# Kernel tuning notes

Measured on AMD Instinct MI355X. Metric: run time of the kernel, lower is better.

Reference implementation:

```python
import jax, jax.numpy as jnp
import numpy as np

NUM_HEADS = 16


def setup_inputs() -> dict:
    key = jax.random.key(0)
    ks = jax.random.split(key, 7)
    B, S, H = 4, 2048, 1024
    scale = 1.0 / np.sqrt(H)
    return {
        "hidden_states": jax.random.normal(ks[0], (B, S, H), dtype=jnp.float32),
        "attention_mask": jnp.ones((B, S), dtype=jnp.int32),
        "Wq": jax.random.normal(ks[1], (H, H), dtype=jnp.float32) * scale,
        "bq": jnp.zeros((H,), dtype=jnp.float32),
        "Wk": jax.random.normal(ks[2], (H, H), dtype=jnp.float32) * scale,
        "bk": jnp.zeros((H,), dtype=jnp.float32),
        "Wv": jax.random.normal(ks[3], (H, H), dtype=jnp.float32) * scale,
        "bv": jnp.zeros((H,), dtype=jnp.float32),
    }


def _split_heads(x, n_heads):
    B, S, H = x.shape
    return x.reshape(B, S, n_heads, H // n_heads).transpose(0, 2, 1, 3)  # [B,h,S,d]


def reference(hidden_states, attention_mask, Wq, bq, Wk, bk, Wv, bv):
    B, S, H = hidden_states.shape
    dh = H // NUM_HEADS
    # nn.Linear applies x @ W.T + b
    q = _split_heads(hidden_states @ Wq.T + bq, NUM_HEADS)
    k = _split_heads(hidden_states @ Wk.T + bk, NUM_HEADS)
    v = _split_heads(hidden_states @ Wv.T + bv, NUM_HEADS)
    scores = jnp.einsum("bhqd,bhkd->bhqk", q, k)  # [B,h,S,S]
    # masked_fill with -inf before scaling == masking after scaling
    mask = attention_mask[:, None, None, :] == 0
    scores = jnp.where(mask, -jnp.inf, scores)
    probs = jax.nn.softmax(scores / jnp.sqrt(jnp.float32(dh)), axis=-1)
    out = jnp.einsum("bhqk,bhkd->bhqd", probs, v)  # [B,h,S,d]
    return out.transpose(0, 2, 1, 3).reshape(B, S, H)
```

## Files before the change

### kernel.cpp

```cpp
#include <hip/hip_runtime.h>
#include <hip/hip_bf16.h>
#include <stdint.h>

constexpr int CB  = 4;
constexpr int CS  = 2048;
constexpr int CH  = 1024;
constexpr int CNH = 16;
constexpr int CDH = 64;
constexpr int CM  = CB * CS;

typedef __bf16 bf16x8 __attribute__((ext_vector_type(8)));
typedef float  f32x4  __attribute__((ext_vector_type(4)));

__device__ __forceinline__ unsigned short f2bf(float f) {
    union { float f; unsigned u; } c; c.f = f;
    unsigned u = c.u;
    unsigned r = (u + 0x7fffu + ((u >> 16) & 1u)) >> 16;
    return (unsigned short)r;
}

__device__ __forceinline__ void gl_lds16(const void* g, void* l) {
    __builtin_amdgcn_global_load_lds((const __attribute__((address_space(1))) uint32_t*)g,
                                     (__attribute__((address_space(3))) uint32_t*)l,
                                     16, 0, 0);
}

__device__ __forceinline__ float fexp2(float x) {
#if __has_builtin(__builtin_amdgcn_exp2f)
    return __builtin_amdgcn_exp2f(x);
#else
    return exp2f(x);
#endif
}

__device__ __forceinline__ unsigned vperm(unsigned s0, unsigned s1, unsigned sel) {
#if __has_builtin(__builtin_amdgcn_perm)
    return __builtin_amdgcn_perm(s0, s1, sel);
#else
    unsigned r = 0;
    for (int k = 0; k < 4; k++) {
        unsigned idx = (sel >> (8 * k)) & 0xff;
        unsigned byte = (idx < 4) ? (s1 >> (8 * idx)) : (s0 >> (8 * (idx - 4)));
        r |= (byte & 0xff) << (8 * k);
    }
    return r;
#endif
}
__device__ __forceinline__ unsigned pack_hihalf(unsigned lo_u, unsigned hi_u) {
    return vperm(hi_u, lo_u, 0x07060302u);
}

constexpr float C_SC = 0.125f * 1.44269504f;

__global__ __launch_bounds__(256) void cvt_all(const float* __restrict__ hs,
                                               const float* __restrict__ w0,
                                               const float* __restrict__ w1,
                                               const float* __restrict__ w2,
                                               unsigned short* __restrict__ Xb,
                                               unsigned short* __restrict__ Wb) {
    int z = blockIdx.y;
    const float* src; unsigned short* dst; int n4;
    if (z == 0)      { src = hs; dst = Xb;              n4 = CM * CH / 4; }
    else if (z == 1) { src = w0; dst = Wb;              n4 = CH * CH / 4; }
    else if (z == 2) { src = w1; dst = Wb + CH * CH;    n4 = CH * CH / 4; }
    else             { src = w2; dst = Wb + 2 * CH * CH; n4 = CH * CH / 4; }
    int i = blockIdx.x * blockDim.x + threadIdx.x;
    if (i < n4) {
        float4 v = ((const float4*)src)[i];
        ushort4 o;
        o.x = f2bf(v.x); o.y = f2bf(v.y); o.z = f2bf(v.z); o.w = f2bf(v.w);
        ((ushort4*)dst)[i] = o;
    }
}

__global__ __launch_bounds__(256) void qkv_gemm(
    const unsigned short* __restrict__ Xb,
    const unsigned short* __restrict__ Wb,
    const float* __restrict__ bq, const float* __restrict__ bk, const float* __restrict__ bv,
    unsigned short* __restrict__ Qo,
    unsigned short* __restrict__ Ko,
    unsigned short* __restrict__ Vt)
{
    __shared__ alignas(16) unsigned char smem[34816];
    typedef unsigned short (*tile_t)[128][32];
    tile_t As = (tile_t)smem;
    tile_t Bs = (tile_t)(smem + 16384);
    typedef unsigned short (*ep_t)[136];
    ep_t Ep = (ep_t)smem;

    const int tid  = threadIdx.x;
    const int wave = tid >> 6, lane = tid & 63;
    const int wm = wave >> 1, wn = wave & 1;
    const int col = lane & 15, quad = lane >> 4;
    const int gm = blockIdx.x * 128, gn = blockIdx.y * 128;
    const int z  = blockIdx.z;
    const unsigned short* W = Wb + (size_t)z * CH * CH;

    f32x4 zero = {0.f, 0.f, 0.f, 0.f};
    f32x4 acc[4][4];
    for (int i = 0; i < 4; i++) for (int j = 0; j < 4; j++) acc[i][j] = zero;

    const int arow = lane >> 2;
    const int acol = (lane & 3) * 8;

    auto stage = [&](int buf, int k0) {
        for (int c = 0; c < 2; ++c) {
            int r0 = wave * 32 + c * 16;
            gl_lds16(Xb + (size_t)(gm + r0 + arow) * CH + k0 + acol, &As[buf][r0][0]);
            gl_lds16(W  + (size_t)(gn + r0 + arow) * CH + k0 + acol, &Bs[buf][r0][0]);
        }
    };

    stage(0, 0);
    for (int kk = 0; kk < 32; ++kk) {
        int cur = kk & 1;
        __syncthreads();
        if (kk < 31) stage(cur ^ 1, (kk + 1) * 32);
        bf16x8 af[4], bfm[4];
        for (int i = 0; i < 4; i++)
            af[i] = *(const bf16x8*)&As[cur][wm * 64 + i * 16 + col][quad * 8];
        for (int j = 0; j < 4; j++)
            bfm[j] = *(const bf16x8*)&Bs[cur][wn * 64 + j * 16 + col][quad * 8];
        for (int i = 0; i < 4; i++)
            for (int j = 0; j < 4; j++)
                acc[i][j] = __builtin_amdgcn_mfma_f32_16x16x32_bf16(af[i], bfm[j], acc[i][j], 0, 0, 0);
    }

    __syncthreads();

    const float* bias = (z == 0) ? bq : (z == 1) ? bk : bv;
    const int bb = gm >> 11, ss0 = gm & 2047;
    const int h0 = gn >> 6;

    if (z == 2) {
        for (int j = 0; j < 4; j++) {
            int nl = wn * 64 + j * 16 + col;
            float bias_v = bias[gn + nl];
            for (int i = 0; i < 4; i++) {
                int ml = wm * 64 + i * 16 + quad * 4;
                unsigned d0 = (unsigned)f2bf(acc[i][j][0] + bias_v) |
                              ((unsigned)f2bf(acc[i][j][1] + bias_v) << 16);
                unsigned d1 = (unsigned)f2bf(acc[i][j][2] + bias_v) |
                              ((unsigned)f2bf(acc[i][j][3] + bias_v) << 16);
                *(unsigned*)&Ep[nl][ml]     = d0;
                *(unsigned*)&Ep[nl][ml + 2] = d1;
            }
        }
        __syncthreads();
        for (int p = 0; p < 8; p++) {
            int nl = p * 16 + (tid >> 4);
            int seg = tid & 15;
            uint4 v = *(const uint4*)&Ep[nl][seg * 8];
            int h = h0 + (nl >> 6), d = nl & 63;
            *(uint4*)(Vt + ((size_t)(bb * CNH + h) * CDH + d) * CS + ss0 + seg * 8) = v;
        }
    } else {
        const float mulf = (z == 0) ? C_SC : 1.0f;
        for (int j = 0; j < 4; j++) {
            int nl = wn * 64 + j * 16 + col;
            float bias_v = bias[gn + nl];
            for (int i = 0; i < 4; i++)
                for (int r = 0; r < 4; r++) {
                    int ml = wm * 64 + i * 16 + quad * 4 + r;
                    Ep[ml][nl] = f2bf((acc[i][j][r] + bias_v) * mulf);
                }
        }
        __syncthreads();
        unsigned short* dst01 = (z == 0) ? Qo : Ko;
        for (int p = 0; p < 8; p++) {
            int ml = p * 16 + (tid >> 4);
            int half = (tid >> 3) & 1, seg = tid & 7;
            uint4 v = *(const uint4*)&Ep[ml][half * 64 + seg * 8];
            int h = h0 + half;
            *(uint4*)(dst01 + ((size_t)(bb * CNH + h) * CS + ss0 + ml) * CDH + seg * 8) = v;
        }
    }
}

__global__ __launch_bounds__(256, 2) void flash_attn(
    const unsigned short* __restrict__ Q,
    const unsigned short* __restrict__ K,
    const unsigned short* __restrict__ Vt,
    const int* __restrict__ mask,
    float* __restrict__ out)
{
    __shared__ alignas(16) unsigned short Ks[2][64][64];
    __shared__ alignas(16) unsigned short Vs[2][64][64];
    __shared__ alignas(16) unsigned int   Ps[4][64][32];
    __shared__ unsigned int Mbits[64];

    const int tid  = threadIdx.x;
    const int wave = tid >> 6, lane = tid & 63;
    const int col = lane & 15, quad = lane >> 4;
    const int bh = blockIdx.y;
    const int bI = bh >> 4, hI = bh & 15;
    const int q0 = blockIdx.x * 256 + wave * 64;

    const unsigned short* Qp = Q  + (size_t)bh * CS * CDH;
    const unsigned short* Kp = K  + (size_t)bh * CS * CDH;
    const unsigned short* Vp = Vt + (size_t)bh * CDH * CS;

    {
        const int* mg = mask + bI * CS;
        for (int j = 0; j < 8; j++) {
            int idx = wave * 512 + j * 64 + lane;
            unsigned long long bal = __ballot(mg[idx] != 0);
            if (lane == 0) {
                Mbits[wave * 16 + j * 2]     = (unsigned int)bal;
                Mbits[wave * 16 + j * 2 + 1] = (unsigned int)(bal >> 32);
            }
        }
    }

    bf16x8 aq[4][2];
    for (int i = 0; i < 4; i++)
        for (int ks = 0; ks < 2; ks++)
            aq[i][ks] = *(const bf16x8*)(Qp + (size_t)(q0 + i * 16 + col) * CDH + ks * 32 + quad * 8);

    bf16x8 onesb;
    {
        union { unsigned short u; __bf16 b; } ob; ob.u = 0x3F80;
        for (int j = 0; j < 8; j++) onesb[j] = ob.b;
    }

    f32x4 zero = {0.f, 0.f, 0.f, 0.f};
    f32x4 o[4][4], lfr[4];
    for (int i = 0; i < 4; i++) {
        lfr[i] = zero;
        for (int id = 0; id < 4; id++) o[i][id] = zero;
    }

    const int srow = lane >> 3;
    const int schk = (lane & 7) ^ srow;

    auto stageKV = [&](int buf, int t) {
        const unsigned short* kg = Kp + (size_t)t * 64 * CDH;
        for (int c = 0; c < 2; c++) {
            int r0 = wave * 16 + c * 8;
            gl_lds16(kg + (size_t)(r0 + srow) * CDH + schk * 8, &Ks[buf][r0][0]);
            gl_lds16(Vp + (size_t)(r0 + srow) * CS + t * 64 + schk * 8, &Vs[buf][r0][0]);
        }
    };

    stageKV(0, 0);
    for (int kt = 0; kt < 32; ++kt) {
        int cur = kt & 1;
        __syncthreads();
        if (kt < 31) stageKV(cur ^ 1, kt + 1);

        f32x4 sfr[4][4];
        for (int i = 0; i < 4; i++) for (int ik = 0; ik < 4; ik++) sfr[i][ik] = zero;
        for (int ks = 0; ks < 2; ks++) {
            bf16x8 bkf[4];
            for (int ik = 0; ik < 4; ik++)
                bkf[ik] = *(const bf16x8*)&Ks[cur][ik * 16 + col][((ks * 4 + quad) ^ (col & 7)) * 8];
            for (int i = 0; i < 4; i++)
                for (int ik = 0; ik < 4; ik++)
                    sfr[i][ik] = __builtin_amdgcn_mfma_f32_16x16x32_bf16(aq[i][ks], bkf[ik], sfr[i][ik], 0, 0, 0);
        }

        unsigned int w0 = Mbits[kt * 2], w1 = Mbits[kt * 2 + 1];
        if ((w0 & w1) != 0xFFFFFFFFu) {
            float madd[4];
            madd[0] = ((w0 >> col) & 1u)        ? 0.f : -1.0e30f;
            madd[1] = ((w0 >> (col + 16)) & 1u) ? 0.f : -1.0e30f;
            madd[2] = ((w1 >> col) & 1u)        ? 0.f : -1.0e30f;
            madd[3] = ((w1 >> (col + 16)) & 1u) ? 0.f : -1.0e30f;
            for (int i = 0; i < 4; i++)
                for (int ik = 0; ik < 4; ik++)
                    for (int r = 0; r < 4; r++)
                        sfr[i][ik][r] += madd[ik];
        }

        for (int i = 0; i < 4; i++)
            for (int ik = 0; ik < 2; ik++)
                for (int r = 0; r < 4; r++) {
                    union { float f; unsigned u; } a, b;
                    a.f = fexp2(sfr[i][ik][r]);
                    b.f = fexp2(sfr[i][ik + 2][r]);
                    unsigned dw = pack_hihalf(a.u, b.u);
                    int row = i * 16 + quad * 4 + r;
                    int p = ik * 16 + col;
                    Ps[wave][row][(((p >> 2) ^ (row & 7)) << 2) + (p & 3)] = dw;
                }

        for (int i = 0; i < 4; i++) {
            const unsigned* base = &Ps[wave][i * 16 + col][0];
            uint4 w0v = *(const uint4*)(base + (((quad * 2 + 0) ^ (col & 7)) << 2));
            uint4 w1v = *(const uint4*)(base + (((quad * 2 + 1) ^ (col & 7)) << 2));
            uint4 lo, hi;
            lo.x = vperm(w0v.y, w0v.x, 0x05040100u); hi.x = vperm(w0v.y, w0v.x, 0x07060302u);
            lo.y = vperm(w0v.w, w0v.z, 0x05040100u); hi.y = vperm(w0v.w, w0v.z, 0x07060302u);
            lo.z = vperm(w1v.y, w1v.x, 0x05040100u); hi.z = vperm(w1v.y, w1v.x, 0x07060302u);
            lo.w = vperm(w1v.w, w1v.z, 0x05040100u); hi.w = vperm(w1v.w, w1v.z, 0x07060302u);
            bf16x8 ap0, ap1;
            __builtin_memcpy(&ap0, &lo, 16);
            __builtin_memcpy(&ap1, &hi, 16);

            for (int ks = 0; ks < 2; ks++) {
                bf16x8 ap = (ks == 0) ? ap0 : ap1;
                bf16x8 bvf[4];
                for (int id = 0; id < 4; id++)
                    bvf[id] = *(const bf16x8*)&Vs[cur][id * 16 + col][((ks * 4 + quad) ^ (col & 7)) * 8];
                for (int id = 0; id < 4; id++)
                    o[i][id] = __builtin_amdgcn_mfma_f32_16x16x32_bf16(ap, bvf[id], o[i][id], 0, 0, 0);
                lfr[i] = __builtin_amdgcn_mfma_f32_16x16x32_bf16(ap, onesb, lfr[i], 0, 0, 0);
            }
        }
    }

    for (int i = 0; i < 4; i++)
        for (int r = 0; r < 4; r++) {
            int sI = q0 + i * 16 + quad * 4 + r;
            float inv = 1.0f / lfr[i][r];
            for (int id = 0; id < 4; id++)
                out[((size_t)(bI * CS + sI)) * CH + hI * CDH + id * 16 + col] = o[i][id][r] * inv;
        }
}

extern "C" void kernel_launch(void* const* d_in, const int* in_sizes, int n_in,
                              void* d_out, int out_size, void* d_ws, size_t ws_size,
                              hipStream_t stream) {
    const float* hs  = (const float*)d_in[0];
    const int*  mask = (const int*)d_in[1];
    const float* Wq  = (const float*)d_in[2];
    const float* bq  = (const float*)d_in[3];
    const float* Wk  = (const float*)d_in[4];
    const float* bk  = (const float*)d_in[5];
    const float* Wv  = (const float*)d_in[6];
    const float* bv  = (const float*)d_in[7];
    float* out = (float*)d_out;

    char* ws = (char*)d_ws;
    unsigned short* Xb = (unsigned short*)(ws);
    unsigned short* Wb = (unsigned short*)(ws + 16777216);
    unsigned short* Qb = (unsigned short*)(ws + 23068672);
    unsigned short* Kb = (unsigned short*)(ws + 39845888);
    unsigned short* Vt = (unsigned short*)(ws + 56623104);

    cvt_all<<<dim3(8192, 4), 256, 0, stream>>>(hs, Wq, Wk, Wv, Xb, Wb);

    qkv_gemm<<<dim3(CM / 128, CH / 128, 3), 256, 0, stream>>>(Xb, Wb, bq, bk, bv, Qb, Kb, Vt);

    flash_attn<<<dim3(CS / 256, CB * CNH), 256, 0, stream>>>(Qb, Kb, Vt, mask, out);
}
```

Measured before the change: 262.9 us.

## Transpose QK^T MFMA and build P operand in registers via permlane swaps

The QK^T MFMA operands are swapped so the score tile comes out transposed, with kv indices along rows. Each lane can then pack exp2 results with v_cvt_pk_bf16 and redistribute them with permlane32/16 swaps into the A-operand layout for the PV MFMA. This removes the per-wave LDS round trip through the Ps buffer and the vperm repacking, and frees its shared memory. It also hoists V fragment loads and adds s_setprio around MFMA bursts, at the cost of extra register pressure and reliance on the gfx950 permlane builtins or their slower fallbacks.

Result: faster. 253.6 us (-3.6%).

```diff
diff --git a/kernel.cpp b/kernel.cpp
--- a/kernel.cpp
+++ b/kernel.cpp
@@ -33,21 +33,38 @@
 #endif
 }
 
-__device__ __forceinline__ unsigned vperm(unsigned s0, unsigned s1, unsigned sel) {
-#if __has_builtin(__builtin_amdgcn_perm)
-    return __builtin_amdgcn_perm(s0, s1, sel);
+__device__ __forceinline__ unsigned cvtpk_bf16(float lo, float hi) {
+    unsigned r;
+    asm("v_cvt_pk_bf16_f32 %0, %1, %2" : "=v"(r) : "v"(lo), "v"(hi));
+    return r;
+}
+
+__device__ __forceinline__ void pl32swap(unsigned &a, unsigned &b) {
+#if __has_builtin(__builtin_amdgcn_permlane32_swap)
+    auto r = __builtin_amdgcn_permlane32_swap(a, b, false, false);
+    a = r[0]; b = r[1];
 #else
-    unsigned r = 0;
-    for (int k = 0; k < 4; k++) {
-        unsigned idx = (sel >> (8 * k)) & 0xff;
-        unsigned byte = (idx < 4) ? (s1 >> (8 * idx)) : (s0 >> (8 * (idx - 4)));
-        r |= (byte & 0xff) << (8 * k);
-    }
-    return r;
+    int lane = threadIdx.x & 63;
+    unsigned as = (unsigned)__shfl((int)a, lane ^ 32);
+    unsigned bs = (unsigned)__shfl((int)b, lane ^ 32);
+    unsigned na = (lane < 32) ? a : bs;
+    unsigned nb = (lane < 32) ? as : b;
+    a = na; b = nb;
 #endif
 }
-__device__ __forceinline__ unsigned pack_hihalf(unsigned lo_u, unsigned hi_u) {
-    return vperm(hi_u, lo_u, 0x07060302u);
+
+__device__ __forceinline__ void pl16swap(unsigned &a, unsigned &b) {
+#if __has_builtin(__builtin_amdgcn_permlane16_swap)
+    auto r = __builtin_amdgcn_permlane16_swap(a, b, false, false);
+    a = r[0]; b = r[1];
+#else
+    unsigned as = __builtin_amdgcn_ds_swizzle(a, 0x401F);
+    unsigned bs = __builtin_amdgcn_ds_swizzle(b, 0x401F);
+    int odd = (threadIdx.x >> 4) & 1;
+    unsigned na = odd ? bs : a;
+    unsigned nb = odd ? b : as;
+    a = na; b = nb;
+#endif
 }
 
 constexpr float C_SC = 0.125f * 1.44269504f;
@@ -186,7 +203,6 @@
 {
     __shared__ alignas(16) unsigned short Ks[2][64][64];
     __shared__ alignas(16) unsigned short Vs[2][64][64];
-    __shared__ alignas(16) unsigned int   Ps[4][64][32];
     __shared__ unsigned int Mbits[64];
 
     const int tid  = threadIdx.x;
@@ -254,58 +270,54 @@
             bf16x8 bkf[4];
             for (int ik = 0; ik < 4; ik++)
                 bkf[ik] = *(const bf16x8*)&Ks[cur][ik * 16 + col][((ks * 4 + quad) ^ (col & 7)) * 8];
+            __builtin_amdgcn_s_setprio(1);
             for (int i = 0; i < 4; i++)
                 for (int ik = 0; ik < 4; ik++)
-                    sfr[i][ik] = __builtin_amdgcn_mfma_f32_16x16x32_bf16(aq[i][ks], bkf[ik], sfr[i][ik], 0, 0, 0);
+                    sfr[i][ik] = __builtin_amdgcn_mfma_f32_16x16x32_bf16(bkf[ik], aq[i][ks], sfr[i][ik], 0, 0, 0);
+            __builtin_amdgcn_s_setprio(0);
         }
 
         unsigned int w0 = Mbits[kt * 2], w1 = Mbits[kt * 2 + 1];
         if ((w0 & w1) != 0xFFFFFFFFu) {
-            float madd[4];
-            madd[0] = ((w0 >> col) & 1u)        ? 0.f : -1.0e30f;
-            madd[1] = ((w0 >> (col + 16)) & 1u) ? 0.f : -1.0e30f;
-            madd[2] = ((w1 >> col) & 1u)        ? 0.f : -1.0e30f;
-            madd[3] = ((w1 >> (col + 16)) & 1u) ? 0.f : -1.0e30f;
-            for (int i = 0; i < 4; i++)
-                for (int ik = 0; ik < 4; ik++)
-                    for (int r = 0; r < 4; r++)
-                        sfr[i][ik][r] += madd[ik];
-        }
-
-        for (int i = 0; i < 4; i++)
-            for (int ik = 0; ik < 2; ik++)
+            for (int ik = 0; ik < 4; ik++)
                 for (int r = 0; r < 4; r++) {
-                    union { float f; unsigned u; } a, b;
-                    a.f = fexp2(sfr[i][ik][r]);
-                    b.f = fexp2(sfr[i][ik + 2][r]);
-                    unsigned dw = pack_hihalf(a.u, b.u);
-                    int row = i * 16 + quad * 4 + r;
-                    int p = ik * 16 + col;
-                    Ps[wave][row][(((p >> 2) ^ (row & 7)) << 2) + (p & 3)] = dw;
+                    int kv = ik * 16 + quad * 4 + r;
+                    unsigned bit = (kv < 32) ? (w0 >> kv) : (w1 >> (kv - 32));
+                    float madd = (bit & 1u) ? 0.f : -1.0e30f;
+                    for (int i = 0; i < 4; i++) sfr[i][ik][r] += madd;
                 }
+        }
+
+        bf16x8 bvf[2][4];
+        for (int ks = 0; ks < 2; ks++)
+            for (int id = 0; id < 4; id++)
+                bvf[ks][id] = *(const bf16x8*)&Vs[cur][id * 16 + col][((ks * 4 + quad) ^ (col & 7)) * 8];
 
         for (int i = 0; i < 4; i++) {
-            const unsigned* base = &Ps[wave][i * 16 + col][0];
-            uint4 w0v = *(const uint4*)(base + (((quad * 2 + 0) ^ (col & 7)) << 2));
-            uint4 w1v = *(const uint4*)(base + (((quad * 2 + 1) ^ (col & 7)) << 2));
-            uint4 lo, hi;
-            lo.x = vperm(w0v.y, w0v.x, 0x05040100u); hi.x = vperm(w0v.y, w0v.x, 0x07060302u);
-            lo.y = vperm(w0v.w, w0v.z, 0x05040100u); hi.y = vperm(w0v.w, w0v.z, 0x07060302u);
-            lo.z = vperm(w1v.y, w1v.x, 0x05040100u); hi.z = vperm(w1v.y, w1v.x, 0x07060302u);
-            lo.w = vperm(w1v.w, w1v.z, 0x05040100u); hi.w = vperm(w1v.w, w1v.z, 0x07060302u);
+            unsigned c[4][2];
+            for (int ik = 0; ik < 4; ik++)
+                for (int h = 0; h < 2; h++)
+                    c[ik][h] = cvtpk_bf16(fexp2(sfr[i][ik][2 * h]), fexp2(sfr[i][ik][2 * h + 1]));
+
+            unsigned a0 = c[0][0], b0 = c[1][0]; pl32swap(a0, b0); pl16swap(a0, b0);
+            unsigned a1 = c[0][1], b1 = c[1][1]; pl32swap(a1, b1); pl16swap(a1, b1);
+            unsigned a2 = c[2][0], b2 = c[3][0]; pl32swap(a2, b2); pl16swap(a2, b2);
+            unsigned a3 = c[2][1], b3 = c[3][1]; pl32swap(a3, b3); pl16swap(a3, b3);
+
+            uint4 lo4; lo4.x = a0; lo4.y = a1; lo4.z = b0; lo4.w = b1;
+            uint4 hi4; hi4.x = a2; hi4.y = a3; hi4.z = b2; hi4.w = b3;
             bf16x8 ap0, ap1;
-            __builtin_memcpy(&ap0, &lo, 16);
-            __builtin_memcpy(&ap1, &hi, 16);
-
-            for (int ks = 0; ks < 2; ks++) {
-                bf16x8 ap = (ks == 0) ? ap0 : ap1;
-                bf16x8 bvf[4];
-                for (int id = 0; id < 4; id++)
-                    bvf[id] = *(const bf16x8*)&Vs[cur][id * 16 + col][((ks * 4 + quad) ^ (col & 7)) * 8];
-                for (int id = 0; id < 4; id++)
-                    o[i][id] = __builtin_amdgcn_mfma_f32_16x16x32_bf16(ap, bvf[id], o[i][id], 0, 0, 0);
-                lfr[i] = __builtin_amdgcn_mfma_f32_16x16x32_bf16(ap, onesb, lfr[i], 0, 0, 0);
-            }
+            __builtin_memcpy(&ap0, &lo4, 16);
+            __builtin_memcpy(&ap1, &hi4, 16);
+
+            __builtin_amdgcn_s_setprio(1);
+            for (int id = 0; id < 4; id++)
+                o[i][id] = __builtin_amdgcn_mfma_f32_16x16x32_bf16(ap0, bvf[0][id], o[i][id], 0, 0, 0);
+            lfr[i] = __builtin_amdgcn_mfma_f32_16x16x32_bf16(ap0, onesb, lfr[i], 0, 0, 0);
+            for (int id = 0; id < 4; id++)
+                o[i][id] = __builtin_amdgcn_mfma_f32_16x16x32_bf16(ap1, bvf[1][id], o[i][id], 0, 0, 0);
+            lfr[i] = __builtin_amdgcn_mfma_f32_16x16x32_bf16(ap1, onesb, lfr[i], 0, 0, 0);
+            __builtin_amdgcn_s_setprio(0);
         }
     }
 
```
